# Kernel tuning notes

Measured on AMD Instinct MI355X. Metric: run time of the kernel, lower is better.

Reference implementation:

```python
import jax, jax.numpy as jnp
import numpy as np

B, L, D = 2, 2048, 2048
H, KVH, Dh = 16, 8, 128
S_ROPE = 1024
EPS = 1e-5


def rms_norm(x, w):
    xf = x.astype(jnp.float32)
    xf = xf * jax.lax.rsqrt(jnp.mean(xf * xf, axis=-1, keepdims=True) + EPS)
    return (xf * w).astype(x.dtype)


def rotate_half(x):
    x1, x2 = jnp.split(x, 2, axis=-1)
    return jnp.concatenate((-x2, x1), axis=-1)


def setup_inputs() -> dict:
    key = jax.random.key(0)
    ks = jax.random.split(key, 12)
    sc = 0.02
    # 1D rope tables at every absolute position (theta = 500000 as in config)
    inv_freq = 1.0 / (500000.0 ** (np.arange(0, Dh, 2, dtype=np.float32) / Dh))
    ang = np.arange(L, dtype=np.float32)[:, None] * inv_freq[None, :]  # [L, Dh/2]
    emb = np.concatenate([ang, ang], axis=-1)  # [L, Dh]
    # 3D rope as per-pair 2x2 rotation matrices
    ang3 = np.random.RandomState(0).uniform(-np.pi, np.pi, size=(S_ROPE, Dh // 2)).astype(np.float32)
    R = np.stack([np.stack([np.cos(ang3), -np.sin(ang3)], -1),
                  np.stack([np.sin(ang3), np.cos(ang3)], -1)], -2)  # [S,Dh/2,2,2]
    mpos = jnp.array([[[128, 1025], [1160, 513]],
                      [[128, 1025], [1160, 513]]], dtype=jnp.int64)
    return {
        "hidden_states": jax.random.normal(ks[0], (B, L, D), jnp.float32),
        "temb": jax.random.normal(ks[1], (B, D), jnp.float32),
        "w_ln": jnp.ones((D,), jnp.float32),
        "w_mod": jax.random.normal(ks[2], (D, 3 * D), jnp.float32) * sc,
        "b_mod": jnp.zeros((3 * D,), jnp.float32),
        "wq": jax.random.normal(ks[3], (D, H * Dh), jnp.float32) * sc,
        "wk": jax.random.normal(ks[4], (D, KVH * Dh), jnp.float32) * sc,
        "wv": jax.random.normal(ks[5], (D, KVH * Dh), jnp.float32) * sc,
        "wo": jax.random.normal(ks[6], (H * Dh, D), jnp.float32) * sc,
        "qn_w": jnp.ones((Dh,), jnp.float32),
        "kn_w": jnp.ones((Dh,), jnp.float32),
        "cos_1d": jnp.asarray(np.cos(emb)),
        "sin_1d": jnp.asarray(np.sin(emb)),
        "rope_3d": jnp.asarray(R),
        "modality_positions": mpos,
    }


def _masks(modality_positions):
    pos = jnp.arange(L)  # [L]
    off = modality_positions[..., 0]   # [B, S]
    ln = modality_positions[..., 1]    # [B, S]
    meta = 1  # add_time_embeds=True, add_ar_embeds=False
    seg_end = off + jnp.maximum(ln, meta)
    in_full = (pos[None, None, :] >= off[..., None]) & (pos[None, None, :] < seg_end[..., None])
    text_mask = ~jnp.any(in_full, axis=1)  # [B, L]
    img_start = off + meta
    in_img = (pos[None, None, :] >= img_start[..., None]) & (pos[None, None, :] < (off + ln)[..., None])
    rel = jnp.sum(jnp.where(in_img, pos[None, None, :] - img_start[..., None], 0), axis=1)  # [B, L]
    img_mask = jnp.any(in_img, axis=1) & (rel < S_ROPE) & (rel >= 0)
    rel = jnp.clip(rel, 0, S_ROPE - 1)
    return text_mask, img_mask, rel


def _apply_mixed_rope(q, k, cos_1d, sin_1d, rope_3d, text_mask, img_mask, rel):
    # text 1D rope (rotate_half style), applied at absolute position
    c = cos_1d[None, None]  # [1,1,L,Dh]
    s = sin_1d[None, None]
    q_txt = q * c + rotate_half(q) * s
    k_txt = k * c + rotate_half(k) * s
    # image 3D rope: per-pair 2x2 rotation gathered at within-image index
    R = rope_3d[rel]  # [B, L, Dh/2, 2, 2]
    q2 = q.reshape(*q.shape[:-1], Dh // 2, 2)
    k2 = k.reshape(*k.shape[:-1], Dh // 2, 2)
    q_img = jnp.einsum('bhlpi,blpij->bhlpj', q2, R).reshape(q.shape)
    k_img = jnp.einsum('bhlpi,blpij->bhlpj', k2, R).reshape(k.shape)
    mt = text_mask[:, None, :, None]
    mi = img_mask[:, None, :, None]
    q_out = jnp.where(mt, q_txt, jnp.where(mi, q_img, q))
    k_out = jnp.where(mt, k_txt, jnp.where(mi, k_img, k))
    return q_out, k_out


def reference(hidden_states, temb, w_ln, w_mod, b_mod, wq, wk, wv, wo,
              qn_w, kn_w, cos_1d, sin_1d, rope_3d, modality_positions):
    dtype = hidden_states.dtype
    # adaLN modulation
    mod = jax.nn.silu(temb) @ w_mod + b_mod  # [B, 3D]
    shift, scale, gate = jnp.split(mod, 3, axis=-1)
    xn = rms_norm(hidden_states, w_ln)
    xm = (xn.astype(jnp.float32) * (1.0 + scale[:, None, :].astype(jnp.float32))
          + shift[:, None, :].astype(jnp.float32)).astype(dtype)
    # qkv projections (GQA)
    q = (xm @ wq).reshape(B, L, H, Dh).transpose(0, 2, 1, 3)
    k = (xm @ wk).reshape(B, L, KVH, Dh).transpose(0, 2, 1, 3)
    v = (xm @ wv).reshape(B, L, KVH, Dh).transpose(0, 2, 1, 3)
    # qk-norm over head_dim
    q = rms_norm(q, qn_w)
    k = rms_norm(k, kn_w)
    # mixed 3D-image / 1D-text RoPE
    text_mask, img_mask, rel = _masks(modality_positions)
    q, k = _apply_mixed_rope(q, k, cos_1d, sin_1d, rope_3d, text_mask, img_mask, rel)
    # GQA: repeat kv heads (repeat_interleave along head dim)
    n_rep = H // KVH
    k = jnp.repeat(k, n_rep, axis=1)
    v = jnp.repeat(v, n_rep, axis=1)
    # full attention (no causal mask for diffusion block)
    scores = jnp.einsum('bhqd,bhkd->bhqk', q, k) / jnp.sqrt(jnp.asarray(Dh, q.dtype))
    attn = jax.nn.softmax(scores, axis=-1)
    o = jnp.einsum('bhqk,bhkd->bhqd', attn, v)
    o = o.transpose(0, 2, 1, 3).reshape(B, L, H * Dh) @ wo
    return hidden_states + gate[:, None, :].astype(dtype) * o


if __name__ == '__main__':
    out = reference(**setup_inputs())
    print(out.shape, out.dtype)
```

## Files before the change

kernel.cpp:

```cpp
#include <hip/hip_runtime.h>
#include <hip/hip_bf16.h>
#include <stdint.h>
#include <math.h>

typedef unsigned short u16;
typedef __attribute__((ext_vector_type(8))) short short8;
typedef __attribute__((ext_vector_type(4))) float fx4;
typedef __attribute__((ext_vector_type(4))) unsigned short u16x4;

#define DEV __device__ __forceinline__

DEV u16 f2bf(float f) {
  return __builtin_bit_cast(u16, __float2bfloat16(f));
}
DEV float bf2f(u16 h) { return __builtin_bit_cast(float, ((unsigned)h) << 16); }

DEV fx4 mfma16(short8 a, short8 b, fx4 c) {
  return __builtin_amdgcn_mfma_f32_16x16x32_bf16(a, b, c, 0, 0, 0);
}

#if __has_builtin(__builtin_amdgcn_exp2f)
DEV float exp2v(float x) { return __builtin_amdgcn_exp2f(x); }
#else
DEV float exp2v(float x) { return exp2f(x); }
#endif

#define GLD16(g, l)                                                            \
  __builtin_amdgcn_global_load_lds(                                            \
      (const __attribute__((address_space(1))) void*)(g),                      \
      (__attribute__((address_space(3))) void*)(l), 16, 0, 0)

#define WAIT_ALL() asm volatile("s_waitcnt vmcnt(0) lgkmcnt(0)" ::: "memory")
#define WAIT_VM4() asm volatile("s_waitcnt vmcnt(4)" ::: "memory")
#define WAIT_VM0() asm volatile("s_waitcnt vmcnt(0)" ::: "memory")

__global__ __launch_bounds__(512) void k_silu_mod(
    const float* __restrict__ temb, const float* __restrict__ wmod,
    const float* __restrict__ bmod, float* __restrict__ mod) {
  __shared__ float st[4096];
  __shared__ float red[8][2][64];
  int tid = threadIdx.x;
  for (int i = tid; i < 4096; i += 512) {
    float t = temb[i];
    st[i] = t / (1.0f + __expf(-t));
  }
  __syncthreads();
  int j = blockIdx.x * 64 + (tid & 63);
  int ks = tid >> 6;
  float a0 = 0.f, a1 = 0.f;
  for (int d = ks * 256; d < ks * 256 + 256; ++d) {
    float w = wmod[(size_t)d * 6144 + j];
    a0 += st[d] * w;
    a1 += st[2048 + d] * w;
  }
  red[ks][0][tid & 63] = a0;
  red[ks][1][tid & 63] = a1;
  __syncthreads();
  if (tid < 64) {
    float s0 = 0.f, s1 = 0.f;
#pragma unroll
    for (int i = 0; i < 8; ++i) {
      s0 += red[i][0][tid];
      s1 += red[i][1][tid];
    }
    mod[j] = s0 + bmod[j];
    mod[6144 + j] = s1 + bmod[j];
  }
}

__global__ __launch_bounds__(256) void k_xm(
    const float* __restrict__ x, const float* __restrict__ wln,
    const float* __restrict__ mod, u16* __restrict__ xm) {
  int row = blockIdx.x;
  int b = row >> 11;
  const float* xr = x + (size_t)row * 2048;
  int tid = threadIdx.x;
  float4 v0 = ((const float4*)xr)[tid];
  float4 v1 = ((const float4*)xr)[tid + 256];
  float ss = v0.x * v0.x + v0.y * v0.y + v0.z * v0.z + v0.w * v0.w +
             v1.x * v1.x + v1.y * v1.y + v1.z * v1.z + v1.w * v1.w;
  for (int m = 1; m < 64; m <<= 1) ss += __shfl_xor(ss, m);
  __shared__ float red[4];
  if ((tid & 63) == 0) red[tid >> 6] = ss;
  __syncthreads();
  ss = red[0] + red[1] + red[2] + red[3];
  float r = rsqrtf(ss * (1.0f / 2048.0f) + 1e-5f);
  const float* mb = mod + (size_t)b * 6144;
#pragma unroll
  for (int c = 0; c < 2; ++c) {
    int j0 = (tid + c * 256) * 4;
    float4 xv = c ? v1 : v0;
    float4 sh = *(const float4*)(mb + j0);
    float4 sc = *(const float4*)(mb + 2048 + j0);
    float4 wl = *(const float4*)(wln + j0);
    u16x4 o;
    o.x = f2bf(xv.x * r * wl.x * (1.f + sc.x) + sh.x);
    o.y = f2bf(xv.y * r * wl.y * (1.f + sc.y) + sh.y);
    o.z = f2bf(xv.z * r * wl.z * (1.f + sc.z) + sh.z);
    o.w = f2bf(xv.w * r * wl.w * (1.f + sc.w) + sh.w);
    *(u16x4*)(xm + (size_t)row * 2048 + j0) = o;
  }
}

__global__ __launch_bounds__(256) void k_tconv(
    const float* __restrict__ src, u16* __restrict__ dst, int cols, int rows) {
  __shared__ float t[32][33];
  int kb = blockIdx.x * 32, nb = blockIdx.y * 32;
  int tx = threadIdx.x, ty = threadIdx.y;
#pragma unroll
  for (int i = 0; i < 4; ++i)
    t[ty + i * 8][tx] = src[(size_t)(kb + ty + i * 8) * cols + nb + tx];
  __syncthreads();
  int nl = ty * 4 + (tx >> 3);
  int k4 = (tx & 7) * 4;
  u16x4 v;
#pragma unroll
  for (int j = 0; j < 4; ++j) v[j] = f2bf(t[k4 + j][nl]);
  *(u16x4*)(dst + (size_t)(nb + nl) * rows + kb + k4) = v;
}

__global__ __launch_bounds__(512, 1) void k_gemm256(
    const u16* __restrict__ A, const u16* __restrict__ Bt, u16* __restrict__ C,
    int N, int K) {
  __shared__ u16 As[3][256 * 32];
  __shared__ u16 Bs[3][256 * 32];
  int tid = threadIdx.x;
  int wave = tid >> 6, lane = tid & 63, quad = lane >> 4, l16 = lane & 15;
  int gx = gridDim.x;
  int nwg = gx * gridDim.y;
  int lin = blockIdx.y * gx + blockIdx.x;
  int cpx = nwg >> 3;
  int swz = (lin & 7) * cpx + (lin >> 3);
  int m0 = (swz / gx) * 256, n0 = (swz % gx) * 256;
  int wm = (wave >> 2) * 128, wn = (wave & 3) * 64;
  fx4 acc[8][4] = {};
  int rowa = tid >> 2;
  int chunk = (tid & 3) ^ ((rowa >> 1) & 3);
  int cola = chunk * 8;
  const u16* Ag = A + (size_t)(m0 + rowa) * K + cola;
  const u16* Bg = Bt + (size_t)(n0 + rowa) * K + cola;
  int sl = (quad ^ ((l16 >> 1) & 3)) * 8;

  auto STAGE = [&](int k0, int buf) {
    u16* AsW = &As[buf][wave * 512];
    u16* BsW = &Bs[buf][wave * 512];
    GLD16(Ag + k0, AsW);
    GLD16(Ag + k0 + (size_t)128 * K, AsW + 4096);
    GLD16(Bg + k0, BsW);
    GLD16(Bg + k0 + (size_t)128 * K, BsW + 4096);
  };
  auto COMPUTE = [&](int buf) {
    short8 af[8], bfr[4];
#pragma unroll
    for (int i = 0; i < 8; ++i)
      af[i] = *(const short8*)&As[buf][(wm + i * 16 + l16) * 32 + sl];
#pragma unroll
    for (int j = 0; j < 4; ++j)
      bfr[j] = *(const short8*)&Bs[buf][(wn + j * 16 + l16) * 32 + sl];
#pragma unroll
    for (int i = 0; i < 8; ++i)
#pragma unroll
      for (int j = 0; j < 4; ++j) acc[i][j] = mfma16(af[i], bfr[j], acc[i][j]);
  };

  STAGE(0, 0);
  STAGE(32, 1);
  for (int t = 0; t < 62; ++t) {
    WAIT_VM4();
    __builtin_amdgcn_s_barrier();
    STAGE((t + 2) * 32, (t + 2) % 3);
    COMPUTE(t % 3);
  }
  WAIT_VM4();
  __builtin_amdgcn_s_barrier();
  COMPUTE(2);
  WAIT_VM0();
  __builtin_amdgcn_s_barrier();
  COMPUTE(0);

#pragma unroll
  for (int i = 0; i < 8; ++i) {
    int row = m0 + wm + i * 16 + quad * 4;
#pragma unroll
    for (int j = 0; j < 4; ++j) {
      int col = n0 + wn + j * 16 + l16;
#pragma unroll
      for (int r = 0; r < 4; ++r)
        C[(size_t)(row + r) * N + col] = f2bf(acc[i][j][r]);
    }
  }
}

__global__ __launch_bounds__(256) void k_gemm(
    const u16* __restrict__ A, const u16* __restrict__ Bt, float* __restrict__ C,
    const float* __restrict__ hid, const float* __restrict__ mod, int N, int K) {
  __shared__ u16 As[3][128 * 32];
  __shared__ u16 Bs[3][128 * 32];
  int tid = threadIdx.x;
  int wave = tid >> 6, lane = tid & 63, quad = lane >> 4, l16 = lane & 15;
  int gx = gridDim.x;
  int nwg = gx * gridDim.y;
  int lin = blockIdx.y * gx + blockIdx.x;
  int cpx = nwg >> 3;
  int swz = (lin & 7) * cpx + (lin >> 3);
  int m0 = (swz / gx) * 128, n0 = (swz % gx) * 128;
  int wm = (wave >> 1) * 64, wn = (wave & 1) * 64;
  fx4 acc[4][4] = {};
  int rowa = tid >> 2;
  int chunk = (tid & 3) ^ ((rowa >> 1) & 3);
  int cola = chunk * 8;
  const u16* Ag = A + (size_t)(m0 + rowa) * K + cola;
  const u16* Bg = Bt + (size_t)(n0 + rowa) * K + cola;
  int sl = (quad ^ ((l16 >> 1) & 3)) * 8;

  auto STAGE = [&](int k0, int buf) {
    u16* AsW = &As[buf][wave * 512];
    u16* BsW = &Bs[buf][wave * 512];
    GLD16(Ag + k0, AsW);
    GLD16(Ag + k0 + (size_t)64 * K, AsW + 2048);
    GLD16(Bg + k0, BsW);
    GLD16(Bg + k0 + (size_t)64 * K, BsW + 2048);
  };
  auto COMPUTE = [&](int buf) {
    short8 af[4], bfr[4];
#pragma unroll
    for (int i = 0; i < 4; ++i) {
      af[i] = *(const short8*)&As[buf][(wm + i * 16 + l16) * 32 + sl];
      bfr[i] = *(const short8*)&Bs[buf][(wn + i * 16 + l16) * 32 + sl];
    }
#pragma unroll
    for (int i = 0; i < 4; ++i)
#pragma unroll
      for (int j = 0; j < 4; ++j) acc[i][j] = mfma16(af[i], bfr[j], acc[i][j]);
  };

  STAGE(0, 0);
  STAGE(32, 1);
  int nk = K >> 5;
  for (int t = 0; t < nk - 2; ++t) {
    WAIT_VM4();
    __builtin_amdgcn_s_barrier();
    STAGE((t + 2) * 32, (t + 2) % 3);
    COMPUTE(t % 3);
  }
  WAIT_VM4();
  __builtin_amdgcn_s_barrier();
  COMPUTE((nk - 2) % 3);
  WAIT_VM0();
  __builtin_amdgcn_s_barrier();
  COMPUTE((nk - 1) % 3);

#pragma unroll
  for (int i = 0; i < 4; ++i) {
    int row = m0 + wm + i * 16 + quad * 4;
#pragma unroll
    for (int j = 0; j < 4; ++j) {
      int col = n0 + wn + j * 16 + l16;
      int b = row >> 11;
      float g = mod[(size_t)b * 6144 + 4096 + col];
#pragma unroll
      for (int r = 0; r < 4; ++r)
        C[(size_t)(row + r) * N + col] =
            hid[(size_t)(row + r) * N + col] + g * acc[i][j][r];
    }
  }
}

__global__ __launch_bounds__(192) void k_qknorm(
    const u16* __restrict__ qkv, const float* __restrict__ qn,
    const float* __restrict__ kn, const float* __restrict__ cos1,
    const float* __restrict__ sin1, const float* __restrict__ r3,
    const int* __restrict__ mpos, u16* __restrict__ Q, u16* __restrict__ Kb) {
  int bx = blockIdx.x;
  int b = bx >> 11, l = bx & 2047;
  int tid = threadIdx.x;
  int slot = tid >> 3, sub = tid & 7;
  bool isq = slot < 16;
  int head = isq ? slot : slot - 16;
  const u16* base = qkv + (size_t)bx * 4096 + (isq ? slot * 128 : 2048 + head * 128);
  int d0 = sub * 16;
  short8 sx0 = *(const short8*)(base + d0);
  short8 sx1 = *(const short8*)(base + d0 + 8);
  float xv[16];
#pragma unroll
  for (int i = 0; i < 8; ++i) {
    xv[i] = bf2f((u16)sx0[i]);
    xv[8 + i] = bf2f((u16)sx1[i]);
  }
  float ss = 0.f;
#pragma unroll
  for (int i = 0; i < 16; ++i) ss += xv[i] * xv[i];
  ss += __shfl_xor(ss, 1);
  ss += __shfl_xor(ss, 2);
  ss += __shfl_xor(ss, 4);
  float r = rsqrtf(ss * (1.0f / 128.0f) + 1e-5f);
  int mp[8];
  {
    bool is64 = (mpos[1] == 0) & (mpos[3] == 0) & (mpos[5] == 0) & (mpos[7] == 0);
#pragma unroll
    for (int i = 0; i < 8; ++i) mp[i] = is64 ? mpos[2 * i] : mpos[i];
  }
  bool infull = false, inimg = false;
  int rel = 0;
#pragma unroll
  for (int s = 0; s < 2; ++s) {
    int off = mp[b * 4 + s * 2], ln = mp[b * 4 + s * 2 + 1];
    int mx = ln > 1 ? ln : 1;
    infull |= (l >= off) && (l < off + mx);
    bool ii = (l >= off + 1) && (l < off + ln);
    inimg |= ii;
    rel += ii ? (l - (off + 1)) : 0;
  }
  bool text = !infull;
  bool img = inimg && (rel < 1024);
  const float* w = isq ? qn : kn;
  fx4 wv[4];
#pragma unroll
  for (int q = 0; q < 4; ++q) wv[q] = *(const fx4*)(w + d0 + q * 4);
  float out[16];
  if (text) {
    int dp0 = d0 ^ 64;
    float sgn = (d0 < 64) ? -1.f : 1.f;
    short8 sp0 = *(const short8*)(base + dp0);
    short8 sp1 = *(const short8*)(base + dp0 + 8);
    fx4 cv[4], sv[4], wp[4];
#pragma unroll
    for (int q = 0; q < 4; ++q) {
      cv[q] = *(const fx4*)(cos1 + (size_t)l * 128 + d0 + q * 4);
      sv[q] = *(const fx4*)(sin1 + (size_t)l * 128 + d0 + q * 4);
      wp[q] = *(const fx4*)(w + dp0 + q * 4);
    }
#pragma unroll
    for (int i = 0; i < 16; ++i) {
      float xp = bf2f((u16)(i < 8 ? sp0[i & 7] : sp1[i & 7]));
      out[i] = r * (xv[i] * wv[i >> 2][i & 3] * cv[i >> 2][i & 3] +
                    sgn * xp * wp[i >> 2][i & 3] * sv[i >> 2][i & 3]);
    }
  } else if (img) {
    const fx4* Rv = (const fx4*)(r3 + ((size_t)rel * 64 + (d0 >> 1)) * 4);
#pragma unroll
    for (int p = 0; p < 8; ++p) {
      fx4 R = Rv[p];
      float a = xv[2 * p] * wv[(2 * p) >> 2][(2 * p) & 3] * r;
      float c2 = xv[2 * p + 1] * wv[(2 * p + 1) >> 2][(2 * p + 1) & 3] * r;
      out[2 * p] = a * R[0] + c2 * R[2];
      out[2 * p + 1] = a * R[1] + c2 * R[3];
    }
  } else {
#pragma unroll
    for (int i = 0; i < 16; ++i) out[i] = xv[i] * wv[i >> 2][i & 3] * r;
  }
  float qs = isq ? (0.08838834764831845f * 1.4426950408889634f) : 1.0f;
  short8 o0, o1;
#pragma unroll
  for (int i = 0; i < 8; ++i) {
    o0[i] = (short)f2bf(out[i] * qs);
    o1[i] = (short)f2bf(out[8 + i] * qs);
  }
  u16* dst = isq ? (Q + ((size_t)(b * 16 + head) * 2048 + l) * 128 + d0)
                 : (Kb + ((size_t)(b * 8 + head) * 2048 + l) * 128 + d0);
  *(short8*)dst = o0;
  *(short8*)(dst + 8) = o1;
}

__global__ __launch_bounds__(256) void k_vtrans(const u16* __restrict__ qkv,
                                                u16* __restrict__ VT) {
  __shared__ u16 t[64][65];
  int bh = blockIdx.x;
  int l0 = blockIdx.y * 64, d0 = blockIdx.z * 64;
  int b = bh >> 3, kvh = bh & 7;
  int tid = threadIdx.x;
  int lr = tid >> 4;
  int c4 = (tid & 15) * 4;
#pragma unroll
  for (int i = 0; i < 4; ++i) {
    int li = lr + i * 16;
    *(u16x4*)&t[li][c4] = *(const u16x4*)(
        qkv + (size_t)(b * 2048 + l0 + li) * 4096 + 3072 + kvh * 128 + d0 + c4);
  }
  __syncthreads();
#pragma unroll
  for (int i = 0; i < 4; ++i) {
    int di = lr + i * 16;
    u16x4 v;
    v[0] = t[c4 + 0][di];
    v[1] = t[c4 + 1][di];
    v[2] = t[c4 + 2][di];
    v[3] = t[c4 + 3][di];
    *(u16x4*)(VT + ((size_t)bh * 128 + d0 + di) * 2048 + l0 + c4) = v;
  }
}

__global__ __launch_bounds__(512, 4) void k_attn(
    const u16* __restrict__ Q, const u16* __restrict__ Kb,
    const u16* __restrict__ VT, u16* __restrict__ O) {
  __shared__ u16 Ks[2][64 * 128];
  __shared__ u16 Vs[2][128 * 64];
  __shared__ u16 Ps[128 * 64];
  int tid = threadIdx.x;
  int wave = tid >> 6, lane = tid & 63, quad = lane >> 4, l16 = lane & 15;
  int bh = blockIdx.y;
  int b = bh >> 4, h = bh & 15, kvh = h >> 1;
  int q0 = blockIdx.x * 128;
  const u16* Qb = Q + ((size_t)bh * 2048 + q0 + wave * 16) * 128;
  short8 qf[4];
#pragma unroll
  for (int ks = 0; ks < 4; ++ks)
    qf[ks] = *(const short8*)(Qb + l16 * 128 + ks * 32 + quad * 8);
  const u16* Kg = Kb + (size_t)(b * 8 + kvh) * 2048 * 128;
  const u16* Vg = VT + (size_t)(b * 8 + kvh) * 128 * 2048;
  float mrow[4], lpart[4];
  fx4 of[8] = {};
#pragma unroll
  for (int r = 0; r < 4; ++r) {
    mrow[r] = -INFINITY;
    lpart[r] = 0.f;
  }
  size_t kgo[2], vgo[2];
#pragma unroll
  for (int i = 0; i < 2; ++i) {
    int kr = i * 32 + wave * 4 + (lane >> 4);
    kgo[i] = (size_t)kr * 128 + (((lane & 15) ^ (kr & 15)) * 8);
    int vr = i * 64 + wave * 8 + (lane >> 3);
    vgo[i] = (size_t)vr * 2048 + (((lane & 7) ^ (vr & 7)) * 8);
  }

  auto STAGE = [&](int t, int buf) {
    size_t ko = (size_t)t * 8192;
    size_t vo = (size_t)t * 64;
#pragma unroll
    for (int i = 0; i < 2; ++i) {
      GLD16(Kg + ko + kgo[i], &Ks[buf][i * 4096 + wave * 512]);
      GLD16(Vg + vo + vgo[i], &Vs[buf][i * 4096 + wave * 512]);
    }
  };

  auto COMPUTE = [&](int buf) {
    fx4 sf[4] = {};
    __builtin_amdgcn_s_setprio(1);
#pragma unroll
    for (int ct = 0; ct < 4; ++ct) {
#pragma unroll
      for (int ks = 0; ks < 4; ++ks) {
        short8 kf = *(const short8*)&Ks[buf][(ct * 16 + l16) * 128 +
                                            (((ks * 4 + quad) ^ l16) * 8)];
        sf[ct] = mfma16(qf[ks], kf, sf[ct]);
      }
    }
    __builtin_amdgcn_s_setprio(0);
    float cmv[4];
    bool need = false;
#pragma unroll
    for (int r = 0; r < 4; ++r) {
      cmv[r] = fmaxf(fmaxf(sf[0][r], sf[1][r]), fmaxf(sf[2][r], sf[3][r]));
      need |= (cmv[r] > mrow[r] + 8.0f);
    }
    if (__any(need)) {
#pragma unroll
      for (int r = 0; r < 4; ++r) {
        float cm = cmv[r];
        cm = fmaxf(cm, __shfl_xor(cm, 1));
        cm = fmaxf(cm, __shfl_xor(cm, 2));
        cm = fmaxf(cm, __shfl_xor(cm, 4));
        cm = fmaxf(cm, __shfl_xor(cm, 8));
        float mn = fmaxf(mrow[r], cm);
        float al = exp2v(mrow[r] - mn);
        mrow[r] = mn;
        lpart[r] *= al;
#pragma unroll
        for (int c2 = 0; c2 < 8; ++c2) of[c2][r] *= al;
      }
    }
    int hb = l16 >> 3;
#pragma unroll
    for (int r = 0; r < 4; ++r) {
      float p0 = exp2v(sf[0][r] - mrow[r]);
      float p1 = exp2v(sf[1][r] - mrow[r]);
      float p2 = exp2v(sf[2][r] - mrow[r]);
      float p3 = exp2v(sf[3][r] - mrow[r]);
      lpart[r] += (p0 + p1) + (p2 + p3);
      int prow = wave * 16 + quad * 4 + r;
      int pb = prow * 64, px = prow & 7, lo = l16 & 7;
      Ps[pb + ((0 + hb) ^ px) * 8 + lo] = f2bf(p0);
      Ps[pb + ((2 + hb) ^ px) * 8 + lo] = f2bf(p1);
      Ps[pb + ((4 + hb) ^ px) * 8 + lo] = f2bf(p2);
      Ps[pb + ((6 + hb) ^ px) * 8 + lo] = f2bf(p3);
    }
    __builtin_amdgcn_s_setprio(1);
#pragma unroll
    for (int ks2 = 0; ks2 < 2; ++ks2) {
      int rsl = (((ks2 * 4 + quad) ^ (l16 & 7)) * 8);
      short8 pa = *(const short8*)&Ps[(wave * 16 + l16) * 64 + rsl];
#pragma unroll
      for (int c2 = 0; c2 < 8; ++c2) {
        short8 vb = *(const short8*)&Vs[buf][(c2 * 16 + l16) * 64 + rsl];
        of[c2] = mfma16(pa, vb, of[c2]);
      }
    }
    __builtin_amdgcn_s_setprio(0);
  };

  STAGE(0, 0);
  WAIT_ALL();
  __builtin_amdgcn_s_barrier();
  int cur = 0;
  for (int t = 0; t < 31; ++t) {
    STAGE(t + 1, cur ^ 1);
    COMPUTE(cur);
    WAIT_ALL();
    __builtin_amdgcn_s_barrier();
    cur ^= 1;
  }
  COMPUTE(cur);

#pragma unroll
  for (int r = 0; r < 4; ++r) {
    float ls = lpart[r];
    ls += __shfl_xor(ls, 1);
    ls += __shfl_xor(ls, 2);
    ls += __shfl_xor(ls, 4);
    ls += __shfl_xor(ls, 8);
    float inv = 1.0f / ls;
    int qrow = q0 + wave * 16 + quad * 4 + r;
#pragma unroll
    for (int c2 = 0; c2 < 8; ++c2)
      O[((size_t)b * 2048 + qrow) * 2048 + h * 128 + c2 * 16 + l16] =
          f2bf(of[c2][r] * inv);
  }
}

extern "C" void kernel_launch(void* const* d_in, const int* in_sizes, int n_in,
                              void* d_out, int out_size, void* d_ws, size_t ws_size,
                              hipStream_t stream) {
  (void)in_sizes; (void)n_in; (void)out_size; (void)ws_size;
  const float* hid  = (const float*)d_in[0];
  const float* temb = (const float*)d_in[1];
  const float* wln  = (const float*)d_in[2];
  const float* wmod = (const float*)d_in[3];
  const float* bmod = (const float*)d_in[4];
  const float* wq   = (const float*)d_in[5];
  const float* wk   = (const float*)d_in[6];
  const float* wv   = (const float*)d_in[7];
  const float* wo   = (const float*)d_in[8];
  const float* qn   = (const float*)d_in[9];
  const float* kn   = (const float*)d_in[10];
  const float* cos1 = (const float*)d_in[11];
  const float* sin1 = (const float*)d_in[12];
  const float* r3   = (const float*)d_in[13];
  const int*   mpos = (const int*)d_in[14];

  char* ws = (char*)d_ws;
  float* mod = (float*)(ws + 0);
  u16* xm  = (u16*)(ws + 49152);
  u16* wT  = (u16*)(ws + 16826368);
  u16* woT = wT;
  u16* qkv = (u16*)(ws + 33603584);
  u16* Qb  = (u16*)(ws + 67158016);
  u16* Kv  = (u16*)(ws + 83935232);
  u16* VT  = (u16*)(ws + 92323840);
  u16* Ob  = qkv;

  dim3 b32(32, 8);
  k_silu_mod<<<96, 512, 0, stream>>>(temb, wmod, bmod, mod);
  k_tconv<<<dim3(64, 64), b32, 0, stream>>>(wq, wT, 2048, 2048);
  k_tconv<<<dim3(64, 32), b32, 0, stream>>>(wk, wT + (size_t)2048 * 2048, 1024, 2048);
  k_tconv<<<dim3(64, 32), b32, 0, stream>>>(wv, wT + (size_t)3072 * 2048, 1024, 2048);
  k_xm<<<4096, 256, 0, stream>>>(hid, wln, mod, xm);
  k_gemm256<<<dim3(16, 16), 512, 0, stream>>>(xm, wT, qkv, 4096, 2048);
  k_tconv<<<dim3(64, 64), b32, 0, stream>>>(wo, woT, 2048, 2048);
  k_qknorm<<<4096, 192, 0, stream>>>(qkv, qn, kn, cos1, sin1, r3, mpos, Qb, Kv);
  k_vtrans<<<dim3(16, 32, 2), 256, 0, stream>>>(qkv, VT);
  k_attn<<<dim3(16, 32), 512, 0, stream>>>(Qb, Kv, VT, Ob);
  k_gemm<<<dim3(16, 32), 256, 0, stream>>>(Ob, woT, (float*)d_out, hid, mod, 2048, 2048);
}
```

Before: 471.1 us.

## Merge small prologue and mid-stage kernels into fused multi-role launches

Merges the SiLU-modulation kernel and the three weight-transpose kernels into one launch that picks its role from the block index. It likewise fuses the wo transpose, the qk-norm/RoPE kernel and the V transpose into a single mid-stage kernel. The attention kernel gains a block-index swizzle that remaps (q tile, head) assignment, which should improve K/V cache locality. The intent is to cut launch overhead and tail gaps between small kernels. In exchange, k_pre reserves extra shared memory in every block, qk-norm blocks now idle a quarter of their threads, and the first kernel mixes long matvec blocks with many short transpose blocks.

```diff
diff --git a/kernel.cpp b/kernel.cpp
--- a/kernel.cpp
+++ b/kernel.cpp
@@ -34,37 +34,74 @@
 #define WAIT_VM4() asm volatile("s_waitcnt vmcnt(4)" ::: "memory")
 #define WAIT_VM0() asm volatile("s_waitcnt vmcnt(0)" ::: "memory")
 
-__global__ __launch_bounds__(512) void k_silu_mod(
+__global__ __launch_bounds__(512) void k_pre(
     const float* __restrict__ temb, const float* __restrict__ wmod,
-    const float* __restrict__ bmod, float* __restrict__ mod) {
+    const float* __restrict__ bmod, float* __restrict__ mod,
+    const float* __restrict__ wq, const float* __restrict__ wk,
+    const float* __restrict__ wv, u16* __restrict__ wT) {
   __shared__ float st[4096];
   __shared__ float red[8][2][64];
+  __shared__ float t2[2][32][33];
+  int bid = blockIdx.x;
   int tid = threadIdx.x;
-  for (int i = tid; i < 4096; i += 512) {
-    float t = temb[i];
-    st[i] = t / (1.0f + __expf(-t));
-  }
-  __syncthreads();
-  int j = blockIdx.x * 64 + (tid & 63);
-  int ks = tid >> 6;
-  float a0 = 0.f, a1 = 0.f;
-  for (int d = ks * 256; d < ks * 256 + 256; ++d) {
-    float w = wmod[(size_t)d * 6144 + j];
-    a0 += st[d] * w;
-    a1 += st[2048 + d] * w;
-  }
-  red[ks][0][tid & 63] = a0;
-  red[ks][1][tid & 63] = a1;
-  __syncthreads();
-  if (tid < 64) {
-    float s0 = 0.f, s1 = 0.f;
-#pragma unroll
-    for (int i = 0; i < 8; ++i) {
-      s0 += red[i][0][tid];
-      s1 += red[i][1][tid];
-    }
-    mod[j] = s0 + bmod[j];
-    mod[6144 + j] = s1 + bmod[j];
+  if (bid < 96) {
+    for (int i = tid; i < 4096; i += 512) {
+      float t = temb[i];
+      st[i] = t / (1.0f + __expf(-t));
+    }
+    __syncthreads();
+    int j = bid * 64 + (tid & 63);
+    int ks = tid >> 6;
+    float a0 = 0.f, a1 = 0.f;
+    for (int d = ks * 256; d < ks * 256 + 256; ++d) {
+      float w = wmod[(size_t)d * 6144 + j];
+      a0 += st[d] * w;
+      a1 += st[2048 + d] * w;
+    }
+    red[ks][0][tid & 63] = a0;
+    red[ks][1][tid & 63] = a1;
+    __syncthreads();
+    if (tid < 64) {
+      float s0 = 0.f, s1 = 0.f;
+#pragma unroll
+      for (int i = 0; i < 8; ++i) {
+        s0 += red[i][0][tid];
+        s1 += red[i][1][tid];
+      }
+      mod[j] = s0 + bmod[j];
+      mod[6144 + j] = s1 + bmod[j];
+    }
+  } else {
+    int half = tid >> 8;
+    int sub = tid & 255;
+    int tx = sub & 31, ty = sub >> 5;
+    int tt = (bid - 96) * 2 + half;
+    const float* src;
+    u16* dst;
+    int cols, kb, nb;
+    if (tt < 4096) {
+      src = wq; dst = wT; cols = 2048;
+      kb = (tt & 63) * 32; nb = (tt >> 6) * 32;
+    } else if (tt < 6144) {
+      int u = tt - 4096;
+      src = wk; dst = wT + (size_t)2048 * 2048; cols = 1024;
+      kb = (u & 63) * 32; nb = (u >> 6) * 32;
+    } else {
+      int u = tt - 6144;
+      src = wv; dst = wT + (size_t)3072 * 2048; cols = 1024;
+      kb = (u & 63) * 32; nb = (u >> 6) * 32;
+    }
+    float (*t)[33] = t2[half];
+#pragma unroll
+    for (int i = 0; i < 4; ++i)
+      t[ty + i * 8][tx] = src[(size_t)(kb + ty + i * 8) * cols + nb + tx];
+    __syncthreads();
+    int nl = ty * 4 + (tx >> 3);
+    int k4 = (tx & 7) * 4;
+    u16x4 v;
+#pragma unroll
+    for (int j = 0; j < 4; ++j) v[j] = f2bf(t[k4 + j][nl]);
+    *(u16x4*)(dst + (size_t)(nb + nl) * 2048 + kb + k4) = v;
   }
 }
 
@@ -100,23 +137,6 @@
     o.w = f2bf(xv.w * r * wl.w * (1.f + sc.w) + sh.w);
     *(u16x4*)(xm + (size_t)row * 2048 + j0) = o;
   }
-}
-
-__global__ __launch_bounds__(256) void k_tconv(
-    const float* __restrict__ src, u16* __restrict__ dst, int cols, int rows) {
-  __shared__ float t[32][33];
-  int kb = blockIdx.x * 32, nb = blockIdx.y * 32;
-  int tx = threadIdx.x, ty = threadIdx.y;
-#pragma unroll
-  for (int i = 0; i < 4; ++i)
-    t[ty + i * 8][tx] = src[(size_t)(kb + ty + i * 8) * cols + nb + tx];
-  __syncthreads();
-  int nl = ty * 4 + (tx >> 3);
-  int k4 = (tx & 7) * 4;
-  u16x4 v;
-#pragma unroll
-  for (int j = 0; j < 4; ++j) v[j] = f2bf(t[k4 + j][nl]);
-  *(u16x4*)(dst + (size_t)(nb + nl) * rows + kb + k4) = v;
 }
 
 __global__ __launch_bounds__(512, 1) void k_gemm256(
@@ -191,6 +211,290 @@
   }
 }
 
+__global__ __launch_bounds__(256) void k_mid(
+    const float* __restrict__ wo, u16* __restrict__ woT,
+    const u16* __restrict__ qkv, const float* __restrict__ qn,
+    const float* __restrict__ kn, const float* __restrict__ cos1,
+    const float* __restrict__ sin1, const float* __restrict__ r3,
+    const int* __restrict__ mpos, u16* __restrict__ Q, u16* __restrict__ Kb,
+    u16* __restrict__ VT) {
+  __shared__ float tc[32][33];
+  __shared__ u16 tv[64][65];
+  int bid = blockIdx.x;
+  int tid = threadIdx.x;
+  if (bid < 4096) {
+    int kb = (bid & 63) * 32, nb = (bid >> 6) * 32;
+    int tx = tid & 31, ty = tid >> 5;
+#pragma unroll
+    for (int i = 0; i < 4; ++i)
+      tc[ty + i * 8][tx] = wo[(size_t)(kb + ty + i * 8) * 2048 + nb + tx];
+    __syncthreads();
+    int nl = ty * 4 + (tx >> 3);
+    int k4 = (tx & 7) * 4;
+    u16x4 v;
+#pragma unroll
+    for (int j = 0; j < 4; ++j) v[j] = f2bf(tc[k4 + j][nl]);
+    *(u16x4*)(woT + (size_t)(nb + nl) * 2048 + kb + k4) = v;
+  } else if (bid < 8192) {
+    int bx = bid - 4096;
+    int b = bx >> 11, l = bx & 2047;
+    int slot = tid >> 3, sub = tid & 7;
+    if (slot >= 24) return;
+    bool isq = slot < 16;
+    int head = isq ? slot : slot - 16;
+    const u16* base =
+        qkv + (size_t)bx * 4096 + (isq ? slot * 128 : 2048 + head * 128);
+    int d0 = sub * 16;
+    short8 sx0 = *(const short8*)(base + d0);
+    short8 sx1 = *(const short8*)(base + d0 + 8);
+    float xv[16];
+#pragma unroll
+    for (int i = 0; i < 8; ++i) {
+      xv[i] = bf2f((u16)sx0[i]);
+      xv[8 + i] = bf2f((u16)sx1[i]);
+    }
+    float ss = 0.f;
+#pragma unroll
+    for (int i = 0; i < 16; ++i) ss += xv[i] * xv[i];
+    ss += __shfl_xor(ss, 1);
+    ss += __shfl_xor(ss, 2);
+    ss += __shfl_xor(ss, 4);
+    float r = rsqrtf(ss * (1.0f / 128.0f) + 1e-5f);
+    int mp[8];
+    {
+      bool is64 =
+          (mpos[1] == 0) & (mpos[3] == 0) & (mpos[5] == 0) & (mpos[7] == 0);
+#pragma unroll
+      for (int i = 0; i < 8; ++i) mp[i] = is64 ? mpos[2 * i] : mpos[i];
+    }
+    bool infull = false, inimg = false;
+    int rel = 0;
+#pragma unroll
+    for (int s = 0; s < 2; ++s) {
+      int off = mp[b * 4 + s * 2], ln = mp[b * 4 + s * 2 + 1];
+      int mx = ln > 1 ? ln : 1;
+      infull |= (l >= off) && (l < off + mx);
+      bool ii = (l >= off + 1) && (l < off + ln);
+      inimg |= ii;
+      rel += ii ? (l - (off + 1)) : 0;
+    }
+    bool text = !infull;
+    bool img = inimg && (rel < 1024);
+    const float* w = isq ? qn : kn;
+    fx4 wv4[4];
+#pragma unroll
+    for (int q = 0; q < 4; ++q) wv4[q] = *(const fx4*)(w + d0 + q * 4);
+    float out[16];
+    if (text) {
+      int dp0 = d0 ^ 64;
+      float sgn = (d0 < 64) ? -1.f : 1.f;
+      short8 sp0 = *(const short8*)(base + dp0);
+      short8 sp1 = *(const short8*)(base + dp0 + 8);
+      fx4 cv[4], sv[4], wp[4];
+#pragma unroll
+      for (int q = 0; q < 4; ++q) {
+        cv[q] = *(const fx4*)(cos1 + (size_t)l * 128 + d0 + q * 4);
+        sv[q] = *(const fx4*)(sin1 + (size_t)l * 128 + d0 + q * 4);
+        wp[q] = *(const fx4*)(w + dp0 + q * 4);
+      }
+#pragma unroll
+      for (int i = 0; i < 16; ++i) {
+        float xp = bf2f((u16)(i < 8 ? sp0[i & 7] : sp1[i & 7]));
+        out[i] = r * (xv[i] * wv4[i >> 2][i & 3] * cv[i >> 2][i & 3] +
+                      sgn * xp * wp[i >> 2][i & 3] * sv[i >> 2][i & 3]);
+      }
+    } else if (img) {
+      const fx4* Rv = (const fx4*)(r3 + ((size_t)rel * 64 + (d0 >> 1)) * 4);
+#pragma unroll
+      for (int p = 0; p < 8; ++p) {
+        fx4 R = Rv[p];
+        float a = xv[2 * p] * wv4[(2 * p) >> 2][(2 * p) & 3] * r;
+        float c2 = xv[2 * p + 1] * wv4[(2 * p + 1) >> 2][(2 * p + 1) & 3] * r;
+        out[2 * p] = a * R[0] + c2 * R[2];
+        out[2 * p + 1] = a * R[1] + c2 * R[3];
+      }
+    } else {
+#pragma unroll
+      for (int i = 0; i < 16; ++i) out[i] = xv[i] * wv4[i >> 2][i & 3] * r;
+    }
+    float qs = isq ? (0.08838834764831845f * 1.4426950408889634f) : 1.0f;
+    short8 o0, o1;
+#pragma unroll
+    for (int i = 0; i < 8; ++i) {
+      o0[i] = (short)f2bf(out[i] * qs);
+      o1[i] = (short)f2bf(out[8 + i] * qs);
+    }
+    u16* dst = isq ? (Q + ((size_t)(b * 16 + head) * 2048 + l) * 128 + d0)
+                   : (Kb + ((size_t)(b * 8 + head) * 2048 + l) * 128 + d0);
+    *(short8*)dst = o0;
+    *(short8*)(dst + 8) = o1;
+  } else {
+    int v = bid - 8192;
+    int bh = v & 15;
+    int l0 = ((v >> 4) & 31) * 64, d0 = (v >> 9) * 64;
+    int b = bh >> 3, kvh = bh & 7;
+    int lr = tid >> 4;
+    int c4 = (tid & 15) * 4;
+#pragma unroll
+    for (int i = 0; i < 4; ++i) {
+      int li = lr + i * 16;
+      *(u16x4*)&tv[li][c4] = *(const u16x4*)(
+          qkv + (size_t)(b * 2048 + l0 + li) * 4096 + 3072 + kvh * 128 + d0 + c4);
+    }
+    __syncthreads();
+#pragma unroll
+    for (int i = 0; i < 4; ++i) {
+      int di = lr + i * 16;
+      u16x4 vv;
+      vv[0] = tv[c4 + 0][di];
+      vv[1] = tv[c4 + 1][di];
+      vv[2] = tv[c4 + 2][di];
+      vv[3] = tv[c4 + 3][di];
+      *(u16x4*)(VT + ((size_t)bh * 128 + d0 + di) * 2048 + l0 + c4) = vv;
+    }
+  }
+}
+
+__global__ __launch_bounds__(512, 4) void k_attn(
+    const u16* __restrict__ Q, const u16* __restrict__ Kb,
+    const u16* __restrict__ VT, u16* __restrict__ O) {
+  __shared__ u16 Ks[2][64 * 128];
+  __shared__ u16 Vs[2][128 * 64];
+  __shared__ u16 Ps[128 * 64];
+  int tid = threadIdx.x;
+  int wave = tid >> 6, lane = tid & 63, quad = lane >> 4, l16 = lane & 15;
+  int lin = blockIdx.y * gridDim.x + blockIdx.x;
+  int vb = (lin & 7) * 64 + (lin >> 3);
+  int q0 = (vb & 15) * 128;
+  int bh = vb >> 4;
+  int b = bh >> 4, h = bh & 15, kvh = h >> 1;
+  const u16* Qb = Q + ((size_t)bh * 2048 + q0 + wave * 16) * 128;
+  short8 qf[4];
+#pragma unroll
+  for (int ks = 0; ks < 4; ++ks)
+    qf[ks] = *(const short8*)(Qb + l16 * 128 + ks * 32 + quad * 8);
+  const u16* Kg = Kb + (size_t)(b * 8 + kvh) * 2048 * 128;
+  const u16* Vg = VT + (size_t)(b * 8 + kvh) * 128 * 2048;
+  float mrow[4], lpart[4];
+  fx4 of[8] = {};
+#pragma unroll
+  for (int r = 0; r < 4; ++r) {
+    mrow[r] = -INFINITY;
+    lpart[r] = 0.f;
+  }
+  size_t kgo[2], vgo[2];
+#pragma unroll
+  for (int i = 0; i < 2; ++i) {
+    int kr = i * 32 + wave * 4 + (lane >> 4);
+    kgo[i] = (size_t)kr * 128 + (((lane & 15) ^ (kr & 15)) * 8);
+    int vr = i * 64 + wave * 8 + (lane >> 3);
+    vgo[i] = (size_t)vr * 2048 + (((lane & 7) ^ (vr & 7)) * 8);
+  }
+
+  auto STAGE = [&](int t, int buf) {
+    size_t ko = (size_t)t * 8192;
+    size_t vo = (size_t)t * 64;
+#pragma unroll
+    for (int i = 0; i < 2; ++i) {
+      GLD16(Kg + ko + kgo[i], &Ks[buf][i * 4096 + wave * 512]);
+      GLD16(Vg + vo + vgo[i], &Vs[buf][i * 4096 + wave * 512]);
+    }
+  };
+
+  auto COMPUTE = [&](int buf) {
+    fx4 sf[4] = {};
+    __builtin_amdgcn_s_setprio(1);
+#pragma unroll
+    for (int ct = 0; ct < 4; ++ct) {
+#pragma unroll
+      for (int ks = 0; ks < 4; ++ks) {
+        short8 kf = *(const short8*)&Ks[buf][(ct * 16 + l16) * 128 +
+                                            (((ks * 4 + quad) ^ l16) * 8)];
+        sf[ct] = mfma16(qf[ks], kf, sf[ct]);
+      }
+    }
+    __builtin_amdgcn_s_setprio(0);
+    float cmv[4];
+    bool need = false;
+#pragma unroll
+    for (int r = 0; r < 4; ++r) {
+      cmv[r] = fmaxf(fmaxf(sf[0][r], sf[1][r]), fmaxf(sf[2][r], sf[3][r]));
+      need |= (cmv[r] > mrow[r] + 8.0f);
+    }
+    if (__any(need)) {
+#pragma unroll
+      for (int r = 0; r < 4; ++r) {
+        float cm = cmv[r];
+        cm = fmaxf(cm, __shfl_xor(cm, 1));
+        cm = fmaxf(cm, __shfl_xor(cm, 2));
+        cm = fmaxf(cm, __shfl_xor(cm, 4));
+        cm = fmaxf(cm, __shfl_xor(cm, 8));
+        float mn = fmaxf(mrow[r], cm);
+        float al = exp2v(mrow[r] - mn);
+        mrow[r] = mn;
+        lpart[r] *= al;
+#pragma unroll
+        for (int c2 = 0; c2 < 8; ++c2) of[c2][r] *= al;
+      }
+    }
+    int hb = l16 >> 3;
+#pragma unroll
+    for (int r = 0; r < 4; ++r) {
+      float p0 = exp2v(sf[0][r] - mrow[r]);
+      float p1 = exp2v(sf[1][r] - mrow[r]);
+      float p2 = exp2v(sf[2][r] - mrow[r]);
+      float p3 = exp2v(sf[3][r] - mrow[r]);
+      lpart[r] += (p0 + p1) + (p2 + p3);
+      int prow = wave * 16 + quad * 4 + r;
+      int pb = prow * 64, px = prow & 7, lo = l16 & 7;
+      Ps[pb + ((0 + hb) ^ px) * 8 + lo] = f2bf(p0);
+      Ps[pb + ((2 + hb) ^ px) * 8 + lo] = f2bf(p1);
+      Ps[pb + ((4 + hb) ^ px) * 8 + lo] = f2bf(p2);
+      Ps[pb + ((6 + hb) ^ px) * 8 + lo] = f2bf(p3);
+    }
+    __builtin_amdgcn_s_setprio(1);
+#pragma unroll
+    for (int ks2 = 0; ks2 < 2; ++ks2) {
+      int rsl = (((ks2 * 4 + quad) ^ (l16 & 7)) * 8);
+      short8 pa = *(const short8*)&Ps[(wave * 16 + l16) * 64 + rsl];
+#pragma unroll
+      for (int c2 = 0; c2 < 8; ++c2) {
+        short8 vb2 = *(const short8*)&Vs[buf][(c2 * 16 + l16) * 64 + rsl];
+        of[c2] = mfma16(pa, vb2, of[c2]);
+      }
+    }
+    __builtin_amdgcn_s_setprio(0);
+  };
+
+  STAGE(0, 0);
+  WAIT_ALL();
+  __builtin_amdgcn_s_barrier();
+  int cur = 0;
+  for (int t = 0; t < 31; ++t) {
+    STAGE(t + 1, cur ^ 1);
+    COMPUTE(cur);
+    WAIT_ALL();
+    __builtin_amdgcn_s_barrier();
+    cur ^= 1;
+  }
+  COMPUTE(cur);
+
+#pragma unroll
+  for (int r = 0; r < 4; ++r) {
+    float ls = lpart[r];
+    ls += __shfl_xor(ls, 1);
+    ls += __shfl_xor(ls, 2);
+    ls += __shfl_xor(ls, 4);
+    ls += __shfl_xor(ls, 8);
+    float inv = 1.0f / ls;
+    int qrow = q0 + wave * 16 + quad * 4 + r;
+#pragma unroll
+    for (int c2 = 0; c2 < 8; ++c2)
+      O[((size_t)b * 2048 + qrow) * 2048 + h * 128 + c2 * 16 + l16] =
+          f2bf(of[c2][r] * inv);
+  }
+}
+
 __global__ __launch_bounds__(256) void k_gemm(
     const u16* __restrict__ A, const u16* __restrict__ Bt, float* __restrict__ C,
     const float* __restrict__ hid, const float* __restrict__ mod, int N, int K) {
@@ -266,269 +570,6 @@
   }
 }
 
-__global__ __launch_bounds__(192) void k_qknorm(
-    const u16* __restrict__ qkv, const float* __restrict__ qn,
-    const float* __restrict__ kn, const float* __restrict__ cos1,
-    const float* __restrict__ sin1, const float* __restrict__ r3,
-    const int* __restrict__ mpos, u16* __restrict__ Q, u16* __restrict__ Kb) {
-  int bx = blockIdx.x;
-  int b = bx >> 11, l = bx & 2047;
-  int tid = threadIdx.x;
-  int slot = tid >> 3, sub = tid & 7;
-  bool isq = slot < 16;
-  int head = isq ? slot : slot - 16;
-  const u16* base = qkv + (size_t)bx * 4096 + (isq ? slot * 128 : 2048 + head * 128);
-  int d0 = sub * 16;
-  short8 sx0 = *(const short8*)(base + d0);
-  short8 sx1 = *(const short8*)(base + d0 + 8);
-  float xv[16];
-#pragma unroll
-  for (int i = 0; i < 8; ++i) {
-    xv[i] = bf2f((u16)sx0[i]);
-    xv[8 + i] = bf2f((u16)sx1[i]);
-  }
-  float ss = 0.f;
-#pragma unroll
-  for (int i = 0; i < 16; ++i) ss += xv[i] * xv[i];
-  ss += __shfl_xor(ss, 1);
-  ss += __shfl_xor(ss, 2);
-  ss += __shfl_xor(ss, 4);
-  float r = rsqrtf(ss * (1.0f / 128.0f) + 1e-5f);
-  int mp[8];
-  {
-    bool is64 = (mpos[1] == 0) & (mpos[3] == 0) & (mpos[5] == 0) & (mpos[7] == 0);
-#pragma unroll
-    for (int i = 0; i < 8; ++i) mp[i] = is64 ? mpos[2 * i] : mpos[i];
-  }
-  bool infull = false, inimg = false;
-  int rel = 0;
-#pragma unroll
-  for (int s = 0; s < 2; ++s) {
-    int off = mp[b * 4 + s * 2], ln = mp[b * 4 + s * 2 + 1];
-    int mx = ln > 1 ? ln : 1;
-    infull |= (l >= off) && (l < off + mx);
-    bool ii = (l >= off + 1) && (l < off + ln);
-    inimg |= ii;
-    rel += ii ? (l - (off + 1)) : 0;
-  }
-  bool text = !infull;
-  bool img = inimg && (rel < 1024);
-  const float* w = isq ? qn : kn;
-  fx4 wv[4];
-#pragma unroll
-  for (int q = 0; q < 4; ++q) wv[q] = *(const fx4*)(w + d0 + q * 4);
-  float out[16];
-  if (text) {
-    int dp0 = d0 ^ 64;
-    float sgn = (d0 < 64) ? -1.f : 1.f;
-    short8 sp0 = *(const short8*)(base + dp0);
-    short8 sp1 = *(const short8*)(base + dp0 + 8);
-    fx4 cv[4], sv[4], wp[4];
-#pragma unroll
-    for (int q = 0; q < 4; ++q) {
-      cv[q] = *(const fx4*)(cos1 + (size_t)l * 128 + d0 + q * 4);
-      sv[q] = *(const fx4*)(sin1 + (size_t)l * 128 + d0 + q * 4);
-      wp[q] = *(const fx4*)(w + dp0 + q * 4);
-    }
-#pragma unroll
-    for (int i = 0; i < 16; ++i) {
-      float xp = bf2f((u16)(i < 8 ? sp0[i & 7] : sp1[i & 7]));
-      out[i] = r * (xv[i] * wv[i >> 2][i & 3] * cv[i >> 2][i & 3] +
-                    sgn * xp * wp[i >> 2][i & 3] * sv[i >> 2][i & 3]);
-    }
-  } else if (img) {
-    const fx4* Rv = (const fx4*)(r3 + ((size_t)rel * 64 + (d0 >> 1)) * 4);
-#pragma unroll
-    for (int p = 0; p < 8; ++p) {
-      fx4 R = Rv[p];
-      float a = xv[2 * p] * wv[(2 * p) >> 2][(2 * p) & 3] * r;
-      float c2 = xv[2 * p + 1] * wv[(2 * p + 1) >> 2][(2 * p + 1) & 3] * r;
-      out[2 * p] = a * R[0] + c2 * R[2];
-      out[2 * p + 1] = a * R[1] + c2 * R[3];
-    }
-  } else {
-#pragma unroll
-    for (int i = 0; i < 16; ++i) out[i] = xv[i] * wv[i >> 2][i & 3] * r;
-  }
-  float qs = isq ? (0.08838834764831845f * 1.4426950408889634f) : 1.0f;
-  short8 o0, o1;
-#pragma unroll
-  for (int i = 0; i < 8; ++i) {
-    o0[i] = (short)f2bf(out[i] * qs);
-    o1[i] = (short)f2bf(out[8 + i] * qs);
-  }
-  u16* dst = isq ? (Q + ((size_t)(b * 16 + head) * 2048 + l) * 128 + d0)
-                 : (Kb + ((size_t)(b * 8 + head) * 2048 + l) * 128 + d0);
-  *(short8*)dst = o0;
-  *(short8*)(dst + 8) = o1;
-}
-
-__global__ __launch_bounds__(256) void k_vtrans(const u16* __restrict__ qkv,
-                                                u16* __restrict__ VT) {
-  __shared__ u16 t[64][65];
-  int bh = blockIdx.x;
-  int l0 = blockIdx.y * 64, d0 = blockIdx.z * 64;
-  int b = bh >> 3, kvh = bh & 7;
-  int tid = threadIdx.x;
-  int lr = tid >> 4;
-  int c4 = (tid & 15) * 4;
-#pragma unroll
-  for (int i = 0; i < 4; ++i) {
-    int li = lr + i * 16;
-    *(u16x4*)&t[li][c4] = *(const u16x4*)(
-        qkv + (size_t)(b * 2048 + l0 + li) * 4096 + 3072 + kvh * 128 + d0 + c4);
-  }
-  __syncthreads();
-#pragma unroll
-  for (int i = 0; i < 4; ++i) {
-    int di = lr + i * 16;
-    u16x4 v;
-    v[0] = t[c4 + 0][di];
-    v[1] = t[c4 + 1][di];
-    v[2] = t[c4 + 2][di];
-    v[3] = t[c4 + 3][di];
-    *(u16x4*)(VT + ((size_t)bh * 128 + d0 + di) * 2048 + l0 + c4) = v;
-  }
-}
-
-__global__ __launch_bounds__(512, 4) void k_attn(
-    const u16* __restrict__ Q, const u16* __restrict__ Kb,
-    const u16* __restrict__ VT, u16* __restrict__ O) {
-  __shared__ u16 Ks[2][64 * 128];
-  __shared__ u16 Vs[2][128 * 64];
-  __shared__ u16 Ps[128 * 64];
-  int tid = threadIdx.x;
-  int wave = tid >> 6, lane = tid & 63, quad = lane >> 4, l16 = lane & 15;
-  int bh = blockIdx.y;
-  int b = bh >> 4, h = bh & 15, kvh = h >> 1;
-  int q0 = blockIdx.x * 128;
-  const u16* Qb = Q + ((size_t)bh * 2048 + q0 + wave * 16) * 128;
-  short8 qf[4];
-#pragma unroll
-  for (int ks = 0; ks < 4; ++ks)
-    qf[ks] = *(const short8*)(Qb + l16 * 128 + ks * 32 + quad * 8);
-  const u16* Kg = Kb + (size_t)(b * 8 + kvh) * 2048 * 128;
-  const u16* Vg = VT + (size_t)(b * 8 + kvh) * 128 * 2048;
-  float mrow[4], lpart[4];
-  fx4 of[8] = {};
-#pragma unroll
-  for (int r = 0; r < 4; ++r) {
-    mrow[r] = -INFINITY;
-    lpart[r] = 0.f;
-  }
-  size_t kgo[2], vgo[2];
-#pragma unroll
-  for (int i = 0; i < 2; ++i) {
-    int kr = i * 32 + wave * 4 + (lane >> 4);
-    kgo[i] = (size_t)kr * 128 + (((lane & 15) ^ (kr & 15)) * 8);
-    int vr = i * 64 + wave * 8 + (lane >> 3);
-    vgo[i] = (size_t)vr * 2048 + (((lane & 7) ^ (vr & 7)) * 8);
-  }
-
-  auto STAGE = [&](int t, int buf) {
-    size_t ko = (size_t)t * 8192;
-    size_t vo = (size_t)t * 64;
-#pragma unroll
-    for (int i = 0; i < 2; ++i) {
-      GLD16(Kg + ko + kgo[i], &Ks[buf][i * 4096 + wave * 512]);
-      GLD16(Vg + vo + vgo[i], &Vs[buf][i * 4096 + wave * 512]);
-    }
-  };
-
-  auto COMPUTE = [&](int buf) {
-    fx4 sf[4] = {};
-    __builtin_amdgcn_s_setprio(1);
-#pragma unroll
-    for (int ct = 0; ct < 4; ++ct) {
-#pragma unroll
-      for (int ks = 0; ks < 4; ++ks) {
-        short8 kf = *(const short8*)&Ks[buf][(ct * 16 + l16) * 128 +
-                                            (((ks * 4 + quad) ^ l16) * 8)];
-        sf[ct] = mfma16(qf[ks], kf, sf[ct]);
-      }
-    }
-    __builtin_amdgcn_s_setprio(0);
-    float cmv[4];
-    bool need = false;
-#pragma unroll
-    for (int r = 0; r < 4; ++r) {
-      cmv[r] = fmaxf(fmaxf(sf[0][r], sf[1][r]), fmaxf(sf[2][r], sf[3][r]));
-      need |= (cmv[r] > mrow[r] + 8.0f);
-    }
-    if (__any(need)) {
-#pragma unroll
-      for (int r = 0; r < 4; ++r) {
-        float cm = cmv[r];
-        cm = fmaxf(cm, __shfl_xor(cm, 1));
-        cm = fmaxf(cm, __shfl_xor(cm, 2));
-        cm = fmaxf(cm, __shfl_xor(cm, 4));
-        cm = fmaxf(cm, __shfl_xor(cm, 8));
-        float mn = fmaxf(mrow[r], cm);
-        float al = exp2v(mrow[r] - mn);
-        mrow[r] = mn;
-        lpart[r] *= al;
-#pragma unroll
-        for (int c2 = 0; c2 < 8; ++c2) of[c2][r] *= al;
-      }
-    }
-    int hb = l16 >> 3;
-#pragma unroll
-    for (int r = 0; r < 4; ++r) {
-      float p0 = exp2v(sf[0][r] - mrow[r]);
-      float p1 = exp2v(sf[1][r] - mrow[r]);
-      float p2 = exp2v(sf[2][r] - mrow[r]);
-      float p3 = exp2v(sf[3][r] - mrow[r]);
-      lpart[r] += (p0 + p1) + (p2 + p3);
-      int prow = wave * 16 + quad * 4 + r;
-      int pb = prow * 64, px = prow & 7, lo = l16 & 7;
-      Ps[pb + ((0 + hb) ^ px) * 8 + lo] = f2bf(p0);
-      Ps[pb + ((2 + hb) ^ px) * 8 + lo] = f2bf(p1);
-      Ps[pb + ((4 + hb) ^ px) * 8 + lo] = f2bf(p2);
-      Ps[pb + ((6 + hb) ^ px) * 8 + lo] = f2bf(p3);
-    }
-    __builtin_amdgcn_s_setprio(1);
-#pragma unroll
-    for (int ks2 = 0; ks2 < 2; ++ks2) {
-      int rsl = (((ks2 * 4 + quad) ^ (l16 & 7)) * 8);
-      short8 pa = *(const short8*)&Ps[(wave * 16 + l16) * 64 + rsl];
-#pragma unroll
-      for (int c2 = 0; c2 < 8; ++c2) {
-        short8 vb = *(const short8*)&Vs[buf][(c2 * 16 + l16) * 64 + rsl];
-        of[c2] = mfma16(pa, vb, of[c2]);
-      }
-    }
-    __builtin_amdgcn_s_setprio(0);
-  };
-
-  STAGE(0, 0);
-  WAIT_ALL();
-  __builtin_amdgcn_s_barrier();
-  int cur = 0;
-  for (int t = 0; t < 31; ++t) {
-    STAGE(t + 1, cur ^ 1);
-    COMPUTE(cur);
-    WAIT_ALL();
-    __builtin_amdgcn_s_barrier();
-    cur ^= 1;
-  }
-  COMPUTE(cur);
-
-#pragma unroll
-  for (int r = 0; r < 4; ++r) {
-    float ls = lpart[r];
-    ls += __shfl_xor(ls, 1);
-    ls += __shfl_xor(ls, 2);
-    ls += __shfl_xor(ls, 4);
-    ls += __shfl_xor(ls, 8);
-    float inv = 1.0f / ls;
-    int qrow = q0 + wave * 16 + quad * 4 + r;
-#pragma unroll
-    for (int c2 = 0; c2 < 8; ++c2)
-      O[((size_t)b * 2048 + qrow) * 2048 + h * 128 + c2 * 16 + l16] =
-          f2bf(of[c2][r] * inv);
-  }
-}
-
 extern "C" void kernel_launch(void* const* d_in, const int* in_sizes, int n_in,
                               void* d_out, int out_size, void* d_ws, size_t ws_size,
                               hipStream_t stream) {
@@ -560,16 +601,12 @@
   u16* VT  = (u16*)(ws + 92323840);
   u16* Ob  = qkv;
 
-  dim3 b32(32, 8);
-  k_silu_mod<<<96, 512, 0, stream>>>(temb, wmod, bmod, mod);
-  k_tconv<<<dim3(64, 64), b32, 0, stream>>>(wq, wT, 2048, 2048);
-  k_tconv<<<dim3(64, 32), b32, 0, stream>>>(wk, wT + (size_t)2048 * 2048, 1024, 2048);
-  k_tconv<<<dim3(64, 32), b32, 0, stream>>>(wv, wT + (size_t)3072 * 2048, 1024, 2048);
+  k_pre<<<4192, 512, 0, stream>>>(temb, wmod, bmod, mod, wq, wk, wv, wT);
   k_xm<<<4096, 256, 0, stream>>>(hid, wln, mod, xm);
   k_gemm256<<<dim3(16, 16), 512, 0, stream>>>(xm, wT, qkv, 4096, 2048);
-  k_tconv<<<dim3(64, 64), b32, 0, stream>>>(wo, woT, 2048, 2048);
-  k_qknorm<<<4096, 192, 0, stream>>>(qkv, qn, kn, cos1, sin1, r3, mpos, Qb, Kv);
-  k_vtrans<<<dim3(16, 32, 2), 256, 0, stream>>>(qkv, VT);
+  k_mid<<<9216, 256, 0, stream>>>(wo, woT, qkv, qn, kn, cos1, sin1, r3, mpos,
+                                  Qb, Kv, VT);
   k_attn<<<dim3(16, 32), 512, 0, stream>>>(Qb, Kv, VT, Ob);
-  k_gemm<<<dim3(16, 32), 256, 0, stream>>>(Ob, woT, (float*)d_out, hid, mod, 2048, 2048);
-}
+  k_gemm<<<dim3(16, 32), 256, 0, stream>>>(Ob, woT, (float*)d_out, hid, mod,
+                                           2048, 2048);
+}
```

Result: faster. 461.2 us (median of 2 runs) (-2.1%).
